# Optimization experiments

Hardware: AMD Instinct MI355X
Metric: run time of the kernel (lower is better)

The kernel has to match this reference:

```python
import jax, jax.numpy as jnp
import numpy as np

WIDTH = 1024
N_HEADS = 16
EPS = 1e-5


def _layernorm(x, gamma, beta):
    m = jnp.mean(x, axis=-1, keepdims=True)
    v = jnp.mean((x - m) ** 2, axis=-1, keepdims=True)  # unbiased=False
    return (x - m) / jnp.sqrt(v + EPS) * gamma + beta


def setup_inputs() -> dict:
    key = jax.random.key(0)
    ks = jax.random.split(key, 8)
    d = WIDTH
    x = jax.random.normal(ks[0], (4, 1024, d), dtype=jnp.float32)
    # MHA params (torch.rand -> uniform [0,1); scale down for numerical sanity is NOT
    # done in the original, but uniform init matches torch.rand semantics)
    in_project = jax.random.uniform(ks[1], (3 * d, d), dtype=jnp.float32)
    out_project = jax.random.uniform(ks[2], (d, d), dtype=jnp.float32)
    ln1_gamma = jnp.ones((d,), jnp.float32)
    ln1_beta = jnp.zeros((d,), jnp.float32)
    ln2_gamma = jnp.ones((d,), jnp.float32)
    ln2_beta = jnp.zeros((d,), jnp.float32)
    w_up = jax.random.uniform(ks[3], (d, 2 * d), dtype=jnp.float32)
    b_up = jax.random.uniform(ks[4], (2 * d,), dtype=jnp.float32)
    w_down = jax.random.uniform(ks[5], (2 * d, d), dtype=jnp.float32)
    b_down = jax.random.uniform(ks[6], (d,), dtype=jnp.float32)
    return {"x": x, "in_project": in_project, "out_project": out_project,
            "ln1_gamma": ln1_gamma, "ln1_beta": ln1_beta,
            "w_up": w_up, "b_up": b_up, "w_down": w_down, "b_down": b_down,
            "ln2_gamma": ln2_gamma, "ln2_beta": ln2_beta}


def reference(x, in_project, out_project, ln1_gamma, ln1_beta,
              w_up, b_up, w_down, b_down, ln2_gamma, ln2_beta):
    B, S, d = x.shape
    H = N_HEADS
    dh = d // H

    # --- masked_attention(ln_1(x)), attn_mask is None ---
    h = _layernorm(x, ln1_gamma, ln1_beta)
    qkv = h @ in_project.T                       # [B,S,3d]
    qkv = qkv.reshape(B, S, 3, H, dh)            # 3H axis splits as (3, H)
    q, k, v = qkv[:, :, 0], qkv[:, :, 1], qkv[:, :, 2]   # [B,S,H,dh]
    scores = jnp.einsum('bqhd,bkhd->bhqk', q, k) / jnp.sqrt(jnp.float32(dh))
    attn = jax.nn.softmax(scores, axis=-1)       # materialized [B,H,S,S] as in original
    o = jnp.einsum('bhqk,bkhd->bqhd', attn, v).reshape(B, S, d)
    o = o @ out_project                          # note: NOT transposed in original
    x = x + o

    # --- ff(ln_2(x)) ---
    h2 = _layernorm(x, ln2_gamma, ln2_beta)
    ff = jnp.maximum(h2 @ w_up + b_up, 0.0) @ w_down + b_down
    return x + ff
```

## Files before the change

### kernel.cpp

```cpp
#include <hip/hip_runtime.h>
#include <hip/hip_bf16.h>


typedef short bf16x8 __attribute__((ext_vector_type(8)));
typedef float f32x4 __attribute__((ext_vector_type(4)));

__device__ __forceinline__ unsigned short f2bf(float f) {
  unsigned int u = __float_as_uint(f);
  unsigned int r = (u + 0x7fffu + ((u >> 16) & 1u)) >> 16;
  return (unsigned short)r;
}
__device__ __forceinline__ float bf2f(unsigned short h) {
  return __uint_as_float(((unsigned int)h) << 16);
}

__device__ __forceinline__ void gld16(const void* g, void* l) {
  __builtin_amdgcn_global_load_lds(
      (const __attribute__((address_space(1))) unsigned int*)g,
      (__attribute__((address_space(3))) unsigned int*)l, 16, 0, 0);
}


__global__ void cast_split_kernel(const float* __restrict__ in,
                                  unsigned short* __restrict__ hi,
                                  unsigned short* __restrict__ lo, int n) {
  int i = blockIdx.x * blockDim.x + threadIdx.x;
  int stride = gridDim.x * blockDim.x;
  for (; i < n; i += stride) {
    float v = in[i];
    unsigned short h = f2bf(v);
    hi[i] = h;
    lo[i] = f2bf(v - bf2f(h));
  }
}

__global__ void transpose3_kernel(const float* __restrict__ op,
                                  const float* __restrict__ wu,
                                  const float* __restrict__ wd,
                                  unsigned short* __restrict__ oT,
                                  unsigned short* __restrict__ uT,
                                  unsigned short* __restrict__ dT) {
  const float* in;
  unsigned short* out;
  int R, C;
  if (blockIdx.z == 0) { in = op; out = oT; R = 1024; C = 1024; }
  else if (blockIdx.z == 1) { in = wu; out = uT; R = 1024; C = 2048; }
  else { in = wd; out = dT; R = 2048; C = 1024; }
  int bc = blockIdx.x << 5;
  int br = blockIdx.y << 5;
  if (bc >= C || br >= R) return;
  __shared__ float t[32][33];
  int tx = threadIdx.x, ty = threadIdx.y;
#pragma unroll
  for (int i = ty; i < 32; i += 8)
    t[i][tx] = in[(size_t)(br + i) * C + bc + tx];
  __syncthreads();
#pragma unroll
  for (int i = ty; i < 32; i += 8)
    out[(size_t)(bc + i) * R + br + tx] = f2bf(t[tx][i]);
}


template <bool SPLIT>
__global__ __launch_bounds__(256) void ln_kernel(
    const float* __restrict__ x, const float* __restrict__ gamma,
    const float* __restrict__ beta, unsigned short* __restrict__ hi,
    unsigned short* __restrict__ lo) {
  int row = blockIdx.x, tid = threadIdx.x;
  float4 v = ((const float4*)x)[(size_t)row * 256 + tid];
  float s = v.x + v.y + v.z + v.w;
  float ss = v.x * v.x + v.y * v.y + v.z * v.z + v.w * v.w;
#pragma unroll
  for (int off = 32; off; off >>= 1) {
    s += __shfl_xor(s, off);
    ss += __shfl_xor(ss, off);
  }
  __shared__ float red[8];
  int wid = tid >> 6, lane = tid & 63;
  if (lane == 0) { red[wid] = s; red[4 + wid] = ss; }
  __syncthreads();
  s = red[0] + red[1] + red[2] + red[3];
  ss = red[4] + red[5] + red[6] + red[7];
  float mean = s * (1.f / 1024.f);
  float var = ss * (1.f / 1024.f) - mean * mean;
  float inv = rsqrtf(var + 1e-5f);
  float4 g = ((const float4*)gamma)[tid];
  float4 bt = ((const float4*)beta)[tid];
  float y[4];
  y[0] = (v.x - mean) * inv * g.x + bt.x;
  y[1] = (v.y - mean) * inv * g.y + bt.y;
  y[2] = (v.z - mean) * inv * g.z + bt.z;
  y[3] = (v.w - mean) * inv * g.w + bt.w;
  size_t o = (size_t)row * 1024 + tid * 4;
#pragma unroll
  for (int j = 0; j < 4; ++j) {
    unsigned short hb = f2bf(y[j]);
    hi[o + j] = hb;
    if (SPLIT) lo[o + j] = f2bf(y[j] - bf2f(hb));
  }
}


template <bool SPLIT, bool BIAS, bool RESID, bool RELU, bool OUTBF16,
          int OUTMODE>
__global__ __launch_bounds__(256) void gemm_kernel(
    const short* __restrict__ Ah, const short* __restrict__ Al,
    const short* __restrict__ Bh, const short* __restrict__ Bl,
    const float* __restrict__ bias, const float* __restrict__ resid,
    void* __restrict__ outp, int M, int N, int K,
    unsigned short* __restrict__ qh, unsigned short* __restrict__ ql,
    unsigned short* __restrict__ kh, unsigned short* __restrict__ kl,
    unsigned short* __restrict__ vtp) {
  __shared__ short As[2][128 * 32];
  __shared__ short Bs[2][128 * 32];
  __shared__ short As2[SPLIT ? 2 : 1][SPLIT ? 128 * 32 : 8];
  __shared__ short Bs2[SPLIT ? 2 : 1][SPLIT ? 128 * 32 : 8];

  const int tid = threadIdx.x;
  const int lane = tid & 63;
  const int wid = tid >> 6;
  const int wr = (wid >> 1) << 6;
  const int wc = (wid & 1) << 6;
  const int l15 = lane & 15, lh = lane >> 4;
  const int rowBase = blockIdx.y << 7;
  const int colBase = blockIdx.x << 7;

  const int sr = tid >> 2;
  const int sc = (tid & 3) << 3;
  const int soff = sr * 32 + sc;
  const short* Ag = Ah + (size_t)(rowBase + sr) * K + sc;
  const short* Bg = Bh + (size_t)(colBase + sr) * K + sc;
  const short* Ag2 = SPLIT ? Al + (size_t)(rowBase + sr) * K + sc : nullptr;
  const short* Bg2 = SPLIT ? Bl + (size_t)(colBase + sr) * K + sc : nullptr;

  f32x4 acc[4][4];
#pragma unroll
  for (int m = 0; m < 4; ++m)
#pragma unroll
    for (int n = 0; n < 4; ++n) acc[m][n] = (f32x4){0.f, 0.f, 0.f, 0.f};

  const int kT = K >> 5;
  {
    gld16(Ag, &As[0][soff]);
    gld16(Ag + (size_t)64 * K, &As[0][soff + 64 * 32]);
    gld16(Bg, &Bs[0][soff]);
    gld16(Bg + (size_t)64 * K, &Bs[0][soff + 64 * 32]);
    if constexpr (SPLIT) {
      gld16(Ag2, &As2[0][soff]);
      gld16(Ag2 + (size_t)64 * K, &As2[0][soff + 64 * 32]);
      gld16(Bg2, &Bs2[0][soff]);
      gld16(Bg2 + (size_t)64 * K, &Bs2[0][soff + 64 * 32]);
    }
  }

  for (int kt = 0; kt < kT; ++kt) {
    __syncthreads();
    const int cb = kt & 1;
    if (kt + 1 < kT) {
      const int nb = cb ^ 1;
      const int k0 = (kt + 1) << 5;
      gld16(Ag + k0, &As[nb][soff]);
      gld16(Ag + k0 + (size_t)64 * K, &As[nb][soff + 64 * 32]);
      gld16(Bg + k0, &Bs[nb][soff]);
      gld16(Bg + k0 + (size_t)64 * K, &Bs[nb][soff + 64 * 32]);
      if constexpr (SPLIT) {
        gld16(Ag2 + k0, &As2[nb][soff]);
        gld16(Ag2 + k0 + (size_t)64 * K, &As2[nb][soff + 64 * 32]);
        gld16(Bg2 + k0, &Bs2[nb][soff]);
        gld16(Bg2 + k0 + (size_t)64 * K, &Bs2[nb][soff + 64 * 32]);
      }
    }

    const short* Asb = As[cb];
    const short* Bsb = Bs[cb];
    bf16x8 af[4], bfr[4];
#pragma unroll
    for (int m = 0; m < 4; ++m)
      af[m] = *(const bf16x8*)&Asb[(wr + m * 16 + l15) * 32 + lh * 8];
#pragma unroll
    for (int n = 0; n < 4; ++n)
      bfr[n] = *(const bf16x8*)&Bsb[(wc + n * 16 + l15) * 32 + lh * 8];
    if constexpr (SPLIT) {
      const short* Asb2 = As2[cb];
      const short* Bsb2 = Bs2[cb];
      bf16x8 af2[4], bfr2[4];
#pragma unroll
      for (int m = 0; m < 4; ++m)
        af2[m] = *(const bf16x8*)&Asb2[(wr + m * 16 + l15) * 32 + lh * 8];
#pragma unroll
      for (int n = 0; n < 4; ++n)
        bfr2[n] = *(const bf16x8*)&Bsb2[(wc + n * 16 + l15) * 32 + lh * 8];
#pragma unroll
      for (int m = 0; m < 4; ++m)
#pragma unroll
        for (int n = 0; n < 4; ++n) {
          acc[m][n] = __builtin_amdgcn_mfma_f32_16x16x32_bf16(af[m], bfr[n], acc[m][n], 0, 0, 0);
          acc[m][n] = __builtin_amdgcn_mfma_f32_16x16x32_bf16(af[m], bfr2[n], acc[m][n], 0, 0, 0);
          acc[m][n] = __builtin_amdgcn_mfma_f32_16x16x32_bf16(af2[m], bfr[n], acc[m][n], 0, 0, 0);
        }
    } else {
#pragma unroll
      for (int m = 0; m < 4; ++m)
#pragma unroll
        for (int n = 0; n < 4; ++n)
          acc[m][n] = __builtin_amdgcn_mfma_f32_16x16x32_bf16(af[m], bfr[n], acc[m][n], 0, 0, 0);
    }
  }

  const int prow = rowBase + wr + lh * 4;
  const int pcol = colBase + wc + l15;
#pragma unroll
  for (int m = 0; m < 4; ++m) {
#pragma unroll
    for (int n = 0; n < 4; ++n) {
      const int c = pcol + n * 16;
      float badd = 0.f;
      if constexpr (BIAS) badd = bias[c];
#pragma unroll
      for (int i = 0; i < 4; ++i) {
        const int r = prow + m * 16 + i;
        float v = acc[m][n][i] + badd;
        if constexpr (OUTMODE == 1) {
          const int part = c >> 10;
          const int cc = c & 1023;
          const int head = cc >> 6, dim = cc & 63;
          const int b = r >> 10, s = r & 1023;
          size_t idx = (((size_t)(b * 16 + head)) * 1024 + s) * 64 + dim;
          if (part == 0) {
            float y = v * 0.125f;
            unsigned short hb = f2bf(y);
            qh[idx] = hb;
            ql[idx] = f2bf(y - bf2f(hb));
          } else {
            unsigned short hb = f2bf(v);
            kh[idx] = hb;
            kl[idx] = f2bf(v - bf2f(hb));
          }
        } else if constexpr (OUTMODE == 2) {
          const int head = c >> 6, dim = c & 63;
          const int b = r >> 10, s = r & 1023;
          vtp[(((size_t)(b * 16 + head)) * 64 + dim) * 1024 + s] = f2bf(v);
        } else {
          if constexpr (RESID) v += resid[(size_t)r * N + c];
          if constexpr (RELU) v = fmaxf(v, 0.f);
          if constexpr (OUTBF16)
            ((unsigned short*)outp)[(size_t)r * N + c] = f2bf(v);
          else
            ((float*)outp)[(size_t)r * N + c] = v;
        }
      }
    }
  }
}


__global__ __launch_bounds__(512, 2) void attn_mfma_kernel(
    const short* __restrict__ qhi, const short* __restrict__ qlo,
    const short* __restrict__ khi, const short* __restrict__ klo,
    const short* __restrict__ vt, unsigned short* __restrict__ o,
    int S, int H) {
  __shared__ short Kh[2][64 * 64];
  __shared__ short Kl[2][64 * 64];
  __shared__ short Vs[2][64 * 64];
  __shared__ short Pl[8][16 * 66];

  const int tid = threadIdx.x, lane = tid & 63, wid = tid >> 6;
  const int l15 = lane & 15, lh = lane >> 4;
  const int blk = blockIdx.x;
  const int j = blk >> 3;
  const int bh = ((blk & 7) << 3) + (j & 7);
  const int q0 = (j >> 3) << 7;
  const size_t hb = (size_t)bh * S * 64;

  const size_t qrow = hb + (size_t)(q0 + wid * 16 + l15) * 64;
  bf16x8 aqh[2], aql[2];
  aqh[0] = *(const bf16x8*)(qhi + qrow + lh * 8);
  aqh[1] = *(const bf16x8*)(qhi + qrow + 32 + lh * 8);
  aql[0] = *(const bf16x8*)(qlo + qrow + lh * 8);
  aql[1] = *(const bf16x8*)(qlo + qrow + 32 + lh * 8);

  float m_run = -INFINITY, l_run = 0.f;
  f32x4 acc_o[4];
#pragma unroll
  for (int n = 0; n < 4; ++n) acc_o[n] = (f32x4){0.f, 0.f, 0.f, 0.f};

  const int r0 = tid >> 3, c0 = tid & 7;
  const int sw0 = ((c0 ^ (r0 & 7)) << 3);

  const int nT = S >> 6;
  {
    gld16(khi + hb + r0 * 64 + sw0, (char*)Kh[0] + tid * 16);
    gld16(klo + hb + r0 * 64 + sw0, (char*)Kl[0] + tid * 16);
    gld16(vt + hb + (size_t)r0 * S + sw0, (char*)Vs[0] + tid * 16);
  }

  for (int kt = 0; kt < nT; ++kt) {
    __syncthreads();
    const int cb = kt & 1;
    if (kt + 1 < nT) {
      const int nb = cb ^ 1;
      const size_t kb = hb + (size_t)(kt + 1) * 64 * 64;
      gld16(khi + kb + r0 * 64 + sw0, (char*)Kh[nb] + tid * 16);
      gld16(klo + kb + r0 * 64 + sw0, (char*)Kl[nb] + tid * 16);
      const short* vg = vt + hb + (size_t)(kt + 1) * 64;
      gld16(vg + (size_t)r0 * S + sw0, (char*)Vs[nb] + tid * 16);
    }

    const short* KhB = Kh[cb];
    const short* KlB = Kl[cb];
    const short* VsB = Vs[cb];

    f32x4 accs[4];
#pragma unroll
    for (int n = 0; n < 4; ++n) accs[n] = (f32x4){0.f, 0.f, 0.f, 0.f};
    __builtin_amdgcn_s_setprio(1);
#pragma unroll
    for (int n = 0; n < 4; ++n) {
      const int row = n * 16 + l15;
      const int sw = row & 7;
      const int ro = row * 64;
      bf16x8 bh0 = *(const bf16x8*)&KhB[ro + ((lh ^ sw) << 3)];
      bf16x8 bh1 = *(const bf16x8*)&KhB[ro + (((4 + lh) ^ sw) << 3)];
      bf16x8 bl0 = *(const bf16x8*)&KlB[ro + ((lh ^ sw) << 3)];
      bf16x8 bl1 = *(const bf16x8*)&KlB[ro + (((4 + lh) ^ sw) << 3)];
      accs[n] = __builtin_amdgcn_mfma_f32_16x16x32_bf16(bh0, aqh[0], accs[n], 0, 0, 0);
      accs[n] = __builtin_amdgcn_mfma_f32_16x16x32_bf16(bh1, aqh[1], accs[n], 0, 0, 0);
      accs[n] = __builtin_amdgcn_mfma_f32_16x16x32_bf16(bl0, aqh[0], accs[n], 0, 0, 0);
      accs[n] = __builtin_amdgcn_mfma_f32_16x16x32_bf16(bl1, aqh[1], accs[n], 0, 0, 0);
      accs[n] = __builtin_amdgcn_mfma_f32_16x16x32_bf16(bh0, aql[0], accs[n], 0, 0, 0);
      accs[n] = __builtin_amdgcn_mfma_f32_16x16x32_bf16(bh1, aql[1], accs[n], 0, 0, 0);
    }
    __builtin_amdgcn_s_setprio(0);

    float m01 = fmaxf(fmaxf(accs[0][0], accs[0][1]), fmaxf(accs[0][2], accs[0][3]));
    float m11 = fmaxf(fmaxf(accs[1][0], accs[1][1]), fmaxf(accs[1][2], accs[1][3]));
    float m21 = fmaxf(fmaxf(accs[2][0], accs[2][1]), fmaxf(accs[2][2], accs[2][3]));
    float m31 = fmaxf(fmaxf(accs[3][0], accs[3][1]), fmaxf(accs[3][2], accs[3][3]));
    float mt = fmaxf(fmaxf(m01, m11), fmaxf(m21, m31));
    mt = fmaxf(mt, __shfl_xor(mt, 16));
    mt = fmaxf(mt, __shfl_xor(mt, 32));

    if (__any(mt > m_run + 8.f)) {
      float mn = fmaxf(m_run, mt);
      float a = __expf(m_run - mn);
      m_run = mn;
      l_run *= a;
      float a0 = __shfl(a, lh * 4 + 0);
      float a1 = __shfl(a, lh * 4 + 1);
      float a2 = __shfl(a, lh * 4 + 2);
      float a3 = __shfl(a, lh * 4 + 3);
#pragma unroll
      for (int n = 0; n < 4; ++n) {
        acc_o[n][0] *= a0; acc_o[n][1] *= a1;
        acc_o[n][2] *= a2; acc_o[n][3] *= a3;
      }
    }

    short* pw = Pl[wid];
    unsigned int* pw32 = (unsigned int*)pw;
#pragma unroll
    for (int n = 0; n < 4; ++n) {
      float p0 = __expf(accs[n][0] - m_run);
      float p1 = __expf(accs[n][1] - m_run);
      float p2 = __expf(accs[n][2] - m_run);
      float p3 = __expf(accs[n][3] - m_run);
      l_run += (p0 + p1) + (p2 + p3);
      pw32[l15 * 33 + n * 8 + lh * 2 + 0] =
          ((unsigned int)f2bf(p1) << 16) | f2bf(p0);
      pw32[l15 * 33 + n * 8 + lh * 2 + 1] =
          ((unsigned int)f2bf(p3) << 16) | f2bf(p2);
    }

    bf16x8 pa0 = *(const bf16x8*)&pw[l15 * 66 + lh * 8];
    bf16x8 pa1 = *(const bf16x8*)&pw[l15 * 66 + 32 + lh * 8];
    __builtin_amdgcn_s_setprio(1);
#pragma unroll
    for (int n = 0; n < 4; ++n) {
      const int row = n * 16 + l15;
      const int sw = row & 7;
      const int ro = row * 64;
      bf16x8 bv0 = *(const bf16x8*)&VsB[ro + ((lh ^ sw) << 3)];
      bf16x8 bv1 = *(const bf16x8*)&VsB[ro + (((4 + lh) ^ sw) << 3)];
      acc_o[n] = __builtin_amdgcn_mfma_f32_16x16x32_bf16(pa0, bv0, acc_o[n], 0, 0, 0);
      acc_o[n] = __builtin_amdgcn_mfma_f32_16x16x32_bf16(pa1, bv1, acc_o[n], 0, 0, 0);
    }
    __builtin_amdgcn_s_setprio(0);
  }

  float lsum = l_run + __shfl_xor(l_run, 16);
  lsum += __shfl_xor(lsum, 32);
  float lrec = 1.0f / lsum;
  float r0i = __shfl(lrec, lh * 4 + 0);
  float r1i = __shfl(lrec, lh * 4 + 1);
  float r2i = __shfl(lrec, lh * 4 + 2);
  float r3i = __shfl(lrec, lh * 4 + 3);

  const int b = bh >> 4, h = bh & 15;
#pragma unroll
  for (int n = 0; n < 4; ++n) {
    const int dim = n * 16 + l15;
    const float rs[4] = {r0i, r1i, r2i, r3i};
#pragma unroll
    for (int i = 0; i < 4; ++i) {
      const int r = q0 + wid * 16 + lh * 4 + i;
      o[((size_t)(b * S + r)) * 1024 + h * 64 + dim] = f2bf(acc_o[n][i] * rs[i]);
    }
  }
}


extern "C" void kernel_launch(void* const* d_in, const int* in_sizes, int n_in,
                              void* d_out, int out_size, void* d_ws,
                              size_t ws_size, hipStream_t stream) {
  const float* x = (const float*)d_in[0];
  const float* in_project = (const float*)d_in[1];
  const float* out_project = (const float*)d_in[2];
  const float* ln1_g = (const float*)d_in[3];
  const float* ln1_b = (const float*)d_in[4];
  const float* w_up = (const float*)d_in[5];
  const float* b_up = (const float*)d_in[6];
  const float* w_down = (const float*)d_in[7];
  const float* b_down = (const float*)d_in[8];
  const float* ln2_g = (const float*)d_in[9];
  const float* ln2_b = (const float*)d_in[10];

  const int B = in_sizes[0] / (1024 * 1024);
  const int S = 1024, H = 16;
  const int M = B * S;

  char* ws = (char*)d_ws;
  short* h_hi = (short*)(ws + 0);
  short* h_lo = (short*)(ws + 8388608);
  float* x2 = (float*)(ws + 0);
  short* qhi = (short*)(ws + 16777216);
  short* qlo = (short*)(ws + 25165824);
  short* khi = (short*)(ws + 33554432);
  short* klo = (short*)(ws + 41943040);
  short* vt  = (short*)(ws + 50331648);
  short* o = (short*)(ws + 67108864);
  short* h2 = (short*)(ws + 75497472);
  short* u = (short*)(ws + 83886080);
  short* Wq_hi = (short*)(ws + 100663296);
  short* Wq_lo = (short*)(ws + 106954752);
  short* WoT = (short*)(ws + 113246208);
  short* WupT = (short*)(ws + 115343360);
  short* WdnT = (short*)(ws + 119537664);

  cast_split_kernel<<<2048, 256, 0, stream>>>(in_project, (unsigned short*)Wq_hi,
                                              (unsigned short*)Wq_lo, 3072 * 1024);
  transpose3_kernel<<<dim3(64, 64, 3), dim3(32, 8), 0, stream>>>(
      out_project, w_up, w_down, (unsigned short*)WoT, (unsigned short*)WupT,
      (unsigned short*)WdnT);

  ln_kernel<true><<<M, 256, 0, stream>>>(x, ln1_g, ln1_b, (unsigned short*)h_hi,
                                         (unsigned short*)h_lo);

  gemm_kernel<true, false, false, false, false, 1>
      <<<dim3(2048 / 128, M / 128), 256, 0, stream>>>(
          h_hi, h_lo, Wq_hi, Wq_lo, nullptr, nullptr, nullptr, M, 2048, 1024,
          (unsigned short*)qhi, (unsigned short*)qlo, (unsigned short*)khi,
          (unsigned short*)klo, nullptr);

  gemm_kernel<false, false, false, false, false, 2>
      <<<dim3(1024 / 128, M / 128), 256, 0, stream>>>(
          h_hi, nullptr, Wq_hi + (size_t)2048 * 1024, nullptr, nullptr, nullptr,
          nullptr, M, 1024, 1024, nullptr, nullptr, nullptr, nullptr,
          (unsigned short*)vt);

  attn_mfma_kernel<<<512, 512, 0, stream>>>(
      qhi, qlo, khi, klo, vt, (unsigned short*)o, S, H);

  gemm_kernel<false, false, true, false, false, 0>
      <<<dim3(1024 / 128, M / 128), 256, 0, stream>>>(
          o, nullptr, WoT, nullptr, nullptr, x, x2, M, 1024, 1024,
          nullptr, nullptr, nullptr, nullptr, nullptr);

  ln_kernel<false><<<M, 256, 0, stream>>>(x2, ln2_g, ln2_b,
                                          (unsigned short*)h2, nullptr);

  gemm_kernel<false, true, false, true, true, 0>
      <<<dim3(2048 / 128, M / 128), 256, 0, stream>>>(
          h2, nullptr, WupT, nullptr, b_up, nullptr, u, M, 2048, 1024,
          nullptr, nullptr, nullptr, nullptr, nullptr);

  gemm_kernel<false, true, true, false, false, 0>
      <<<dim3(1024 / 128, M / 128), 256, 0, stream>>>(
          u, nullptr, WdnT, nullptr, b_down, x2, d_out, M, 1024, 2048,
          nullptr, nullptr, nullptr, nullptr, nullptr);
}
```

Baseline: 256.4 us.

## Rewrite attention kernel with 32x32 MFMA tiles and register-resident P

Result: no change. 254.3 us (-0.8%).

```diff
diff --git a/kernel.cpp b/kernel.cpp
--- a/kernel.cpp
+++ b/kernel.cpp
@@ -4,6 +4,7 @@
 
 typedef short bf16x8 __attribute__((ext_vector_type(8)));
 typedef float f32x4 __attribute__((ext_vector_type(4)));
+typedef float f32x16 __attribute__((ext_vector_type(16)));
 
 __device__ __forceinline__ unsigned short f2bf(float f) {
   unsigned int u = __float_as_uint(f);
@@ -13,11 +14,36 @@
 __device__ __forceinline__ float bf2f(unsigned short h) {
   return __uint_as_float(((unsigned int)h) << 16);
 }
+__device__ __forceinline__ unsigned pack2(float x, float y) {
+  return ((unsigned)f2bf(y) << 16) | f2bf(x);
+}
 
 __device__ __forceinline__ void gld16(const void* g, void* l) {
   __builtin_amdgcn_global_load_lds(
       (const __attribute__((address_space(1))) unsigned int*)g,
       (__attribute__((address_space(3))) unsigned int*)l, 16, 0, 0);
+}
+
+#if defined(__has_builtin)
+#if __has_builtin(__builtin_amdgcn_permlane32_swap)
+#define HAVE_PLSWAP 1
+#endif
+#endif
+
+__device__ __forceinline__ void plswap(unsigned& a, unsigned& b) {
+#ifdef HAVE_PLSWAP
+  auto r = __builtin_amdgcn_permlane32_swap(a, b, 0, 0);
+  a = r[0];
+  b = r[1];
+#else
+  unsigned ta = (unsigned)__shfl_xor((int)a, 32);
+  unsigned tb = (unsigned)__shfl_xor((int)b, 32);
+  bool hi = (threadIdx.x & 32) != 0;
+  unsigned na = hi ? tb : a;
+  unsigned nb = hi ? b : ta;
+  a = na;
+  b = nb;
+#endif
 }
 
 
@@ -254,7 +280,7 @@
 }
 
 
-__global__ __launch_bounds__(512, 2) void attn_mfma_kernel(
+__global__ __launch_bounds__(256, 2) void attn_mfma_kernel(
     const short* __restrict__ qhi, const short* __restrict__ qlo,
     const short* __restrict__ khi, const short* __restrict__ klo,
     const short* __restrict__ vt, unsigned short* __restrict__ o,
@@ -262,36 +288,42 @@
   __shared__ short Kh[2][64 * 64];
   __shared__ short Kl[2][64 * 64];
   __shared__ short Vs[2][64 * 64];
-  __shared__ short Pl[8][16 * 66];
 
   const int tid = threadIdx.x, lane = tid & 63, wid = tid >> 6;
-  const int l15 = lane & 15, lh = lane >> 4;
+  const int l31 = lane & 31;
+  const int hi = lane >> 5;
   const int blk = blockIdx.x;
   const int j = blk >> 3;
   const int bh = ((blk & 7) << 3) + (j & 7);
   const int q0 = (j >> 3) << 7;
-  const size_t hb = (size_t)bh * S * 64;
-
-  const size_t qrow = hb + (size_t)(q0 + wid * 16 + l15) * 64;
-  bf16x8 aqh[2], aql[2];
-  aqh[0] = *(const bf16x8*)(qhi + qrow + lh * 8);
-  aqh[1] = *(const bf16x8*)(qhi + qrow + 32 + lh * 8);
-  aql[0] = *(const bf16x8*)(qlo + qrow + lh * 8);
-  aql[1] = *(const bf16x8*)(qlo + qrow + 32 + lh * 8);
+  const size_t hbase = (size_t)bh * S * 64;
+
+  const size_t qrow = hbase + (size_t)(q0 + wid * 32 + l31) * 64;
+  bf16x8 qfh[4], qfl[4];
+#pragma unroll
+  for (int t = 0; t < 4; ++t) {
+    qfh[t] = *(const bf16x8*)(qhi + qrow + t * 16 + hi * 8);
+    qfl[t] = *(const bf16x8*)(qlo + qrow + t * 16 + hi * 8);
+  }
 
   float m_run = -INFINITY, l_run = 0.f;
-  f32x4 acc_o[4];
-#pragma unroll
-  for (int n = 0; n < 4; ++n) acc_o[n] = (f32x4){0.f, 0.f, 0.f, 0.f};
+  f32x16 accO0, accO1;
+#pragma unroll
+  for (int r = 0; r < 16; ++r) { accO0[r] = 0.f; accO1[r] = 0.f; }
 
   const int r0 = tid >> 3, c0 = tid & 7;
   const int sw0 = ((c0 ^ (r0 & 7)) << 3);
+  const int r1 = r0 + 32;
+  const int sw1 = ((c0 ^ (r1 & 7)) << 3);
 
   const int nT = S >> 6;
   {
-    gld16(khi + hb + r0 * 64 + sw0, (char*)Kh[0] + tid * 16);
-    gld16(klo + hb + r0 * 64 + sw0, (char*)Kl[0] + tid * 16);
-    gld16(vt + hb + (size_t)r0 * S + sw0, (char*)Vs[0] + tid * 16);
+    gld16(khi + hbase + r0 * 64 + sw0, (char*)Kh[0] + tid * 16);
+    gld16(khi + hbase + r1 * 64 + sw1, (char*)Kh[0] + tid * 16 + 4096);
+    gld16(klo + hbase + r0 * 64 + sw0, (char*)Kl[0] + tid * 16);
+    gld16(klo + hbase + r1 * 64 + sw1, (char*)Kl[0] + tid * 16 + 4096);
+    gld16(vt + hbase + (size_t)r0 * S + sw0, (char*)Vs[0] + tid * 16);
+    gld16(vt + hbase + (size_t)r1 * S + sw1, (char*)Vs[0] + tid * 16 + 4096);
   }
 
   for (int kt = 0; kt < nT; ++kt) {
@@ -299,112 +331,135 @@
     const int cb = kt & 1;
     if (kt + 1 < nT) {
       const int nb = cb ^ 1;
-      const size_t kb = hb + (size_t)(kt + 1) * 64 * 64;
+      const size_t kb = hbase + (size_t)(kt + 1) * 64 * 64;
       gld16(khi + kb + r0 * 64 + sw0, (char*)Kh[nb] + tid * 16);
+      gld16(khi + kb + r1 * 64 + sw1, (char*)Kh[nb] + tid * 16 + 4096);
       gld16(klo + kb + r0 * 64 + sw0, (char*)Kl[nb] + tid * 16);
-      const short* vg = vt + hb + (size_t)(kt + 1) * 64;
+      gld16(klo + kb + r1 * 64 + sw1, (char*)Kl[nb] + tid * 16 + 4096);
+      const short* vg = vt + hbase + (size_t)(kt + 1) * 64;
       gld16(vg + (size_t)r0 * S + sw0, (char*)Vs[nb] + tid * 16);
+      gld16(vg + (size_t)r1 * S + sw1, (char*)Vs[nb] + tid * 16 + 4096);
     }
 
     const short* KhB = Kh[cb];
     const short* KlB = Kl[cb];
     const short* VsB = Vs[cb];
 
-    f32x4 accs[4];
-#pragma unroll
-    for (int n = 0; n < 4; ++n) accs[n] = (f32x4){0.f, 0.f, 0.f, 0.f};
+    f32x16 sA, sB;
+#pragma unroll
+    for (int r = 0; r < 16; ++r) { sA[r] = 0.f; sB[r] = 0.f; }
     __builtin_amdgcn_s_setprio(1);
 #pragma unroll
-    for (int n = 0; n < 4; ++n) {
-      const int row = n * 16 + l15;
-      const int sw = row & 7;
-      const int ro = row * 64;
-      bf16x8 bh0 = *(const bf16x8*)&KhB[ro + ((lh ^ sw) << 3)];
-      bf16x8 bh1 = *(const bf16x8*)&KhB[ro + (((4 + lh) ^ sw) << 3)];
-      bf16x8 bl0 = *(const bf16x8*)&KlB[ro + ((lh ^ sw) << 3)];
-      bf16x8 bl1 = *(const bf16x8*)&KlB[ro + (((4 + lh) ^ sw) << 3)];
-      accs[n] = __builtin_amdgcn_mfma_f32_16x16x32_bf16(bh0, aqh[0], accs[n], 0, 0, 0);
-      accs[n] = __builtin_amdgcn_mfma_f32_16x16x32_bf16(bh1, aqh[1], accs[n], 0, 0, 0);
-      accs[n] = __builtin_amdgcn_mfma_f32_16x16x32_bf16(bl0, aqh[0], accs[n], 0, 0, 0);
-      accs[n] = __builtin_amdgcn_mfma_f32_16x16x32_bf16(bl1, aqh[1], accs[n], 0, 0, 0);
-      accs[n] = __builtin_amdgcn_mfma_f32_16x16x32_bf16(bh0, aql[0], accs[n], 0, 0, 0);
-      accs[n] = __builtin_amdgcn_mfma_f32_16x16x32_bf16(bh1, aql[1], accs[n], 0, 0, 0);
+    for (int t = 0; t < 4; ++t) {
+      const int cA = ((2 * t + hi) ^ (l31 & 7)) << 3;
+      bf16x8 kh0 = *(const bf16x8*)&KhB[l31 * 64 + cA];
+      bf16x8 kl0 = *(const bf16x8*)&KlB[l31 * 64 + cA];
+      bf16x8 kh1 = *(const bf16x8*)&KhB[(32 + l31) * 64 + cA];
+      bf16x8 kl1 = *(const bf16x8*)&KlB[(32 + l31) * 64 + cA];
+      sA = __builtin_amdgcn_mfma_f32_32x32x16_bf16(kh0, qfh[t], sA, 0, 0, 0);
+      sB = __builtin_amdgcn_mfma_f32_32x32x16_bf16(kh1, qfh[t], sB, 0, 0, 0);
+      sA = __builtin_amdgcn_mfma_f32_32x32x16_bf16(kh0, qfl[t], sA, 0, 0, 0);
+      sB = __builtin_amdgcn_mfma_f32_32x32x16_bf16(kh1, qfl[t], sB, 0, 0, 0);
+      sA = __builtin_amdgcn_mfma_f32_32x32x16_bf16(kl0, qfh[t], sA, 0, 0, 0);
+      sB = __builtin_amdgcn_mfma_f32_32x32x16_bf16(kl1, qfh[t], sB, 0, 0, 0);
     }
     __builtin_amdgcn_s_setprio(0);
 
-    float m01 = fmaxf(fmaxf(accs[0][0], accs[0][1]), fmaxf(accs[0][2], accs[0][3]));
-    float m11 = fmaxf(fmaxf(accs[1][0], accs[1][1]), fmaxf(accs[1][2], accs[1][3]));
-    float m21 = fmaxf(fmaxf(accs[2][0], accs[2][1]), fmaxf(accs[2][2], accs[2][3]));
-    float m31 = fmaxf(fmaxf(accs[3][0], accs[3][1]), fmaxf(accs[3][2], accs[3][3]));
-    float mt = fmaxf(fmaxf(m01, m11), fmaxf(m21, m31));
-    mt = fmaxf(mt, __shfl_xor(mt, 16));
-    mt = fmaxf(mt, __shfl_xor(mt, 32));
+    float mt = fmaxf(sA[0], sB[0]);
+#pragma unroll
+    for (int r = 1; r < 16; ++r) mt = fmaxf(mt, fmaxf(sA[r], sB[r]));
+    {
+      unsigned ma = __float_as_uint(mt), mb = ma;
+      plswap(ma, mb);
+      mt = fmaxf(__uint_as_float(ma), __uint_as_float(mb));
+    }
 
     if (__any(mt > m_run + 8.f)) {
       float mn = fmaxf(m_run, mt);
       float a = __expf(m_run - mn);
       m_run = mn;
       l_run *= a;
-      float a0 = __shfl(a, lh * 4 + 0);
-      float a1 = __shfl(a, lh * 4 + 1);
-      float a2 = __shfl(a, lh * 4 + 2);
-      float a3 = __shfl(a, lh * 4 + 3);
-#pragma unroll
-      for (int n = 0; n < 4; ++n) {
-        acc_o[n][0] *= a0; acc_o[n][1] *= a1;
-        acc_o[n][2] *= a2; acc_o[n][3] *= a3;
+#pragma unroll
+      for (int r = 0; r < 16; ++r) {
+        const int qq = (r & 3) + 8 * (r >> 2) + 4 * hi;
+        float ar = __shfl(a, qq);
+        accO0[r] *= ar;
+        accO1[r] *= ar;
       }
     }
 
-    short* pw = Pl[wid];
-    unsigned int* pw32 = (unsigned int*)pw;
-#pragma unroll
-    for (int n = 0; n < 4; ++n) {
-      float p0 = __expf(accs[n][0] - m_run);
-      float p1 = __expf(accs[n][1] - m_run);
-      float p2 = __expf(accs[n][2] - m_run);
-      float p3 = __expf(accs[n][3] - m_run);
-      l_run += (p0 + p1) + (p2 + p3);
-      pw32[l15 * 33 + n * 8 + lh * 2 + 0] =
-          ((unsigned int)f2bf(p1) << 16) | f2bf(p0);
-      pw32[l15 * 33 + n * 8 + lh * 2 + 1] =
-          ((unsigned int)f2bf(p3) << 16) | f2bf(p2);
-    }
-
-    bf16x8 pa0 = *(const bf16x8*)&pw[l15 * 66 + lh * 8];
-    bf16x8 pa1 = *(const bf16x8*)&pw[l15 * 66 + 32 + lh * 8];
+    float pA[16], pB[16];
+#pragma unroll
+    for (int r = 0; r < 16; ++r) {
+      pA[r] = __expf(sA[r] - m_run);
+      pB[r] = __expf(sB[r] - m_run);
+    }
+    float ls = 0.f;
+#pragma unroll
+    for (int r = 0; r < 16; ++r) ls += pA[r] + pB[r];
+    l_run += ls;
+
+    unsigned a0 = pack2(pA[0], pA[1]), a1 = pack2(pA[2], pA[3]);
+    unsigned a2 = pack2(pA[4], pA[5]), a3 = pack2(pA[6], pA[7]);
+    plswap(a0, a2);
+    plswap(a1, a3);
+    unsigned b0 = pack2(pA[8], pA[9]), b1 = pack2(pA[10], pA[11]);
+    unsigned b2 = pack2(pA[12], pA[13]), b3 = pack2(pA[14], pA[15]);
+    plswap(b0, b2);
+    plswap(b1, b3);
+    unsigned c0_ = pack2(pB[0], pB[1]), c1_ = pack2(pB[2], pB[3]);
+    unsigned c2_ = pack2(pB[4], pB[5]), c3_ = pack2(pB[6], pB[7]);
+    plswap(c0_, c2_);
+    plswap(c1_, c3_);
+    unsigned d0 = pack2(pB[8], pB[9]), d1 = pack2(pB[10], pB[11]);
+    unsigned d2 = pack2(pB[12], pB[13]), d3 = pack2(pB[14], pB[15]);
+    plswap(d0, d2);
+    plswap(d1, d3);
+
+    bf16x8 pf0, pf1, pf2, pf3;
+    {
+      unsigned w[4];
+      w[0] = a0; w[1] = a1; w[2] = a2; w[3] = a3;
+      pf0 = *(bf16x8*)w;
+      w[0] = b0; w[1] = b1; w[2] = b2; w[3] = b3;
+      pf1 = *(bf16x8*)w;
+      w[0] = c0_; w[1] = c1_; w[2] = c2_; w[3] = c3_;
+      pf2 = *(bf16x8*)w;
+      w[0] = d0; w[1] = d1; w[2] = d2; w[3] = d3;
+      pf3 = *(bf16x8*)w;
+    }
+
     __builtin_amdgcn_s_setprio(1);
-#pragma unroll
-    for (int n = 0; n < 4; ++n) {
-      const int row = n * 16 + l15;
-      const int sw = row & 7;
-      const int ro = row * 64;
-      bf16x8 bv0 = *(const bf16x8*)&VsB[ro + ((lh ^ sw) << 3)];
-      bf16x8 bv1 = *(const bf16x8*)&VsB[ro + (((4 + lh) ^ sw) << 3)];
-      acc_o[n] = __builtin_amdgcn_mfma_f32_16x16x32_bf16(pa0, bv0, acc_o[n], 0, 0, 0);
-      acc_o[n] = __builtin_amdgcn_mfma_f32_16x16x32_bf16(pa1, bv1, acc_o[n], 0, 0, 0);
+    {
+      const int sw_a = ((l31 & 7)) ;
+      const int d1r = 32 + l31;
+#pragma unroll
+      for (int c = 0; c < 4; ++c) {
+        bf16x8 bv0 = *(const bf16x8*)&VsB[l31 * 64 + ((((2 * c + hi)) ^ (l31 & 7)) << 3)];
+        bf16x8 bv1 = *(const bf16x8*)&VsB[d1r * 64 + ((((2 * c + hi)) ^ (d1r & 7)) << 3)];
+        bf16x8 pf = (c == 0) ? pf0 : (c == 1) ? pf1 : (c == 2) ? pf2 : pf3;
+        accO0 = __builtin_amdgcn_mfma_f32_32x32x16_bf16(pf, bv0, accO0, 0, 0, 0);
+        accO1 = __builtin_amdgcn_mfma_f32_32x32x16_bf16(pf, bv1, accO1, 0, 0, 0);
+      }
     }
     __builtin_amdgcn_s_setprio(0);
   }
 
-  float lsum = l_run + __shfl_xor(l_run, 16);
-  lsum += __shfl_xor(lsum, 32);
-  float lrec = 1.0f / lsum;
-  float r0i = __shfl(lrec, lh * 4 + 0);
-  float r1i = __shfl(lrec, lh * 4 + 1);
-  float r2i = __shfl(lrec, lh * 4 + 2);
-  float r3i = __shfl(lrec, lh * 4 + 3);
+  {
+    unsigned la = __float_as_uint(l_run), lb = la;
+    plswap(la, lb);
+    l_run = __uint_as_float(la) + __uint_as_float(lb);
+  }
+  float lrec = 1.0f / l_run;
 
   const int b = bh >> 4, h = bh & 15;
 #pragma unroll
-  for (int n = 0; n < 4; ++n) {
-    const int dim = n * 16 + l15;
-    const float rs[4] = {r0i, r1i, r2i, r3i};
-#pragma unroll
-    for (int i = 0; i < 4; ++i) {
-      const int r = q0 + wid * 16 + lh * 4 + i;
-      o[((size_t)(b * S + r)) * 1024 + h * 64 + dim] = f2bf(acc_o[n][i] * rs[i]);
-    }
+  for (int r = 0; r < 16; ++r) {
+    const int qq = (r & 3) + 8 * (r >> 2) + 4 * hi;
+    float rr = __shfl(lrec, qq);
+    const size_t row = (size_t)(b * S + q0 + wid * 32 + qq) * 1024 + h * 64;
+    o[row + l31] = f2bf(accO0[r] * rr);
+    o[row + 32 + l31] = f2bf(accO1[r] * rr);
   }
 }
 
@@ -467,7 +522,7 @@
           nullptr, M, 1024, 1024, nullptr, nullptr, nullptr, nullptr,
           (unsigned short*)vt);
 
-  attn_mfma_kernel<<<512, 512, 0, stream>>>(
+  attn_mfma_kernel<<<512, 256, 0, stream>>>(
       qhi, qlo, khi, klo, vt, (unsigned short*)o, S, H);
 
   gemm_kernel<false, false, true, false, false, 0>
```
